# Kernel tuning notes

Measured on AMD Instinct MI355X. Metric: run time of the kernel, lower is better.

The kernel has to match this reference:

```python
import jax, jax.numpy as jnp
import numpy as np

N, F_IN, H, O = 4096, 512, 4, 256
ALPHA = 0.2  # leaky-relu negative slope
NEG = -9e15  # mask value for non-edges (matches DAEGC)


def setup_inputs() -> dict:
    key = jax.random.key(0)
    ks = jax.random.split(key, 9)
    x = jax.random.normal(ks[0], (N, F_IN), jnp.float32)
    adj = (jax.random.uniform(ks[1], (N, N)) < 0.01).astype(jnp.float32)
    adj = jnp.maximum(adj, jnp.eye(N, dtype=jnp.float32))
    M = jax.random.uniform(ks[2], (N, N), dtype=jnp.float32)  # proximity matrix
    s0 = 1.0 / np.sqrt(F_IN)
    s1 = 1.0 / np.sqrt(H * O)
    W0 = jax.random.normal(ks[3], (H, F_IN, O), jnp.float32) * s0
    a_self0 = jax.random.normal(ks[4], (H, O), jnp.float32) * 0.1
    a_neigh0 = jax.random.normal(ks[5], (H, O), jnp.float32) * 0.1
    W1 = jax.random.normal(ks[6], (H, H * O, O), jnp.float32) * s1
    a_self1 = jax.random.normal(ks[7], (H, O), jnp.float32) * 0.1
    a_neigh1 = jax.random.normal(ks[8], (H, O), jnp.float32) * 0.1
    return dict(x=x, adj=adj, M=M, W0=W0, a_self0=a_self0, a_neigh0=a_neigh0,
                W1=W1, a_self1=a_self1, a_neigh1=a_neigh1)


def gat_layer(x, adj, M, W, a_s, a_n, concat):
    # x: [N, F_in], W: [H, F_in, O]
    h = jnp.einsum('nf,hfo->hno', x, W)                      # [H, N, O]
    e = (jnp.einsum('hno,ho->hn', h, a_s)[:, :, None]
         + jnp.einsum('hno,ho->hn', h, a_n)[:, None, :])     # [H, N, N]
    e = jax.nn.leaky_relu(e * M[None], ALPHA)
    e = jnp.where(adj[None] > 0, e, NEG)
    attn = jax.nn.softmax(e, axis=-1)                        # masked neighbor softmax
    out = jnp.einsum('hnm,hmo->hno', attn, h)                # [H, N, O]
    if concat:
        return jax.nn.elu(out.transpose(1, 0, 2).reshape(x.shape[0], -1))  # [N, H*O]
    return out.mean(axis=0)                                  # [N, O]


def reference(x, adj, M, W0, a_self0, a_neigh0, W1, a_self1, a_neigh1):
    h = gat_layer(x, adj, M, W0, a_self0, a_neigh0, True)
    h = gat_layer(h, adj, M, W1, a_self1, a_neigh1, False)
    # F.normalize(h, p=2, dim=1) with eps=1e-12
    z = h / jnp.maximum(jnp.linalg.norm(h, axis=1, keepdims=True), 1e-12)
    A_pred = jax.nn.sigmoid(z @ z.T)                          # dot-product decode [N, N]
    return (A_pred, z)
```

## Files before the change

### kernel.cpp

```cpp
#include <hip/hip_runtime.h>
#include <hip/hip_bf16.h>
#include <math.h>

#define N_NODES 4096
#define F_IN0   512
#define HEADS   4
#define O_DIM   256
#define HO      1024
#define LRELU_A 0.2f
#define MAXE    192
#define LOG2E   1.44269504088896f

typedef __bf16 bf16_t;
typedef bf16_t bf16x8 __attribute__((ext_vector_type(8)));
typedef float f32x4 __attribute__((ext_vector_type(4)));
typedef unsigned short u16x8 __attribute__((ext_vector_type(8)));

__device__ __forceinline__ unsigned short f2b(float f) {
    __hip_bfloat16 t = __float2bfloat16(f);
    return __builtin_bit_cast(unsigned short, t);
}
__device__ __forceinline__ float b2f(unsigned short u) {
    unsigned int v = ((unsigned int)u) << 16;
    return __builtin_bit_cast(float, v);
}
__device__ __forceinline__ float fexp(float x) {
    return __builtin_amdgcn_exp2f(x * LOG2E);
}
__device__ __forceinline__ float fsigmoid(float x) {
    return __builtin_amdgcn_rcpf(1.f + __builtin_amdgcn_exp2f(-x * LOG2E));
}

#define GLOAD_LDS(g, l) \
    __builtin_amdgcn_global_load_lds((const __attribute__((address_space(1))) unsigned int*)(g), \
                                     (__attribute__((address_space(3))) unsigned int*)(l), 16, 0, 0)

__device__ __forceinline__ void transpose_tile(const float* __restrict__ W,
                                               unsigned short* __restrict__ Wt,
                                               int K, int O, int kt, int ot, int h,
                                               float (*t)[33], int tid) {
    const float* Wh = W + (size_t)h * K * O;
    unsigned short* Wth = Wt + (size_t)h * K * O;
    const int k0 = kt * 32, o0 = ot * 32;
    const int tx = tid & 31, ty = tid >> 5;
    for (int r = ty; r < 32; r += 8) t[r][tx] = Wh[(size_t)(k0 + r) * O + o0 + tx];
    __syncthreads();
    for (int r = ty; r < 32; r += 8)
        Wth[(size_t)(o0 + r) * K + k0 + tx] = f2b(t[tx][r]);
}

__global__ __launch_bounds__(256) void prep_k(const float* __restrict__ x,
                                              const float* __restrict__ W0,
                                              const float* __restrict__ W1,
                                              const float* __restrict__ adj,
                                              const float* __restrict__ Mm,
                                              unsigned short* __restrict__ xb,
                                              unsigned short* __restrict__ wt0,
                                              unsigned short* __restrict__ wt1,
                                              int* __restrict__ ecnt,
                                              int* __restrict__ eidx,
                                              float* __restrict__ eMv) {
    __shared__ float t[32][33];
    __shared__ int cnt;
    const int b = blockIdx.x;
    const int tid = threadIdx.x;
    if (b < 2048) {
        int i = b * 256 + tid;
        float4 v = ((const float4*)x)[i];
        ushort4 o;
        o.x = f2b(v.x); o.y = f2b(v.y); o.z = f2b(v.z); o.w = f2b(v.w);
        ((ushort4*)xb)[i] = o;
    } else if (b < 2560) {
        int b2 = b - 2048;
        transpose_tile(W0, wt0, F_IN0, O_DIM, (b2 & 15), ((b2 >> 4) & 7), b2 >> 7, t, tid);
    } else if (b < 3584) {
        int b2 = b - 2560;
        transpose_tile(W1, wt1, HO, O_DIM, (b2 & 31), ((b2 >> 5) & 7), b2 >> 8, t, tid);
    } else {
        const int n = b - 3584;
        if (tid == 0) cnt = 0;
        __syncthreads();
        const float* adjr = adj + (size_t)n * N_NODES;
        const float* Mr   = Mm  + (size_t)n * N_NODES;
        for (int m0 = tid * 4; m0 < N_NODES; m0 += 1024) {
            const float4 a4 = *(const float4*)&adjr[m0];
            const float av[4] = {a4.x, a4.y, a4.z, a4.w};
#pragma unroll
            for (int q = 0; q < 4; ++q) {
                if (av[q] > 0.f) {
                    int m = m0 + q;
                    int k = atomicAdd(&cnt, 1);
                    eidx[(size_t)n * MAXE + k] = m;
                    eMv[(size_t)n * MAXE + k]  = Mr[m];
                }
            }
        }
        __syncthreads();
        if (tid == 0) ecnt[n] = cnt;
    }
}

__global__ __launch_bounds__(256) void mfma_nt(const bf16_t* __restrict__ A,
                                               const bf16_t* __restrict__ B,
                                               unsigned short* __restrict__ Cv,
                                               int K, int ldc,
                                               unsigned long long bStride,
                                               unsigned long long cStride) {
    B += blockIdx.z * bStride;
    const size_t zoff = (size_t)blockIdx.z * cStride;
    __shared__ bf16_t sA[128 * 32];
    __shared__ bf16_t sB[128 * 32];
    const int tid  = threadIdx.x;
    const int lane = tid & 63;
    const int wave = tid >> 6;
    const int wr = (wave >> 1) * 64;
    const int wc = (wave & 1) * 64;
    const int rowBase = blockIdx.x * 128;
    const int colBase = blockIdx.y * 128;
    const int l15  = lane & 15;
    const int quad = lane >> 4;

    const int sm = tid & 127;
    const int sc = tid >> 7;
    const bf16_t* aRow = A + (size_t)(rowBase + sm) * K + sc * 8;
    const bf16_t* bRow = B + (size_t)(colBase + sm) * K + sc * 8;
    bf16_t* sA0 = &sA[(tid & ~63) * 8];
    bf16_t* sA1 = &sA[(256 + (tid & ~63)) * 8];
    bf16_t* sB0 = &sB[(tid & ~63) * 8];
    bf16_t* sB1 = &sB[(256 + (tid & ~63)) * 8];

    f32x4 acc[4][4] = {};

    for (int k0 = 0; k0 < K; k0 += 32) {
        GLOAD_LDS(aRow + k0,      sA0);
        GLOAD_LDS(aRow + k0 + 16, sA1);
        GLOAD_LDS(bRow + k0,      sB0);
        GLOAD_LDS(bRow + k0 + 16, sB1);
        __syncthreads();
        bf16x8 af[4], bfr[4];
#pragma unroll
        for (int i = 0; i < 4; ++i) {
            af[i]  = *(bf16x8*)&sA[(quad * 128 + wr + i * 16 + l15) * 8];
            bfr[i] = *(bf16x8*)&sB[(quad * 128 + wc + i * 16 + l15) * 8];
        }
#pragma unroll
        for (int i = 0; i < 4; ++i)
#pragma unroll
            for (int j = 0; j < 4; ++j)
                acc[i][j] = __builtin_amdgcn_mfma_f32_16x16x32_bf16(af[i], bfr[j], acc[i][j], 0, 0, 0);
        __syncthreads();
    }

    const int orow = rowBase + wr + quad * 4;
    const int ocol = colBase + wc + l15;
#pragma unroll
    for (int i = 0; i < 4; ++i)
#pragma unroll
        for (int j = 0; j < 4; ++j)
#pragma unroll
            for (int r = 0; r < 4; ++r)
                Cv[zoff + (size_t)(orow + i * 16 + r) * ldc + ocol + j * 16] = f2b(acc[i][j][r]);
}

#define EP_STRIDE 132
__global__ __launch_bounds__(256) void decode_k(const bf16_t* __restrict__ Z,
                                                float* __restrict__ out) {
    __shared__ float smem_f[32 * EP_STRIDE];
    bf16_t* sA = (bf16_t*)smem_f;
    bf16_t* sB = (bf16_t*)(smem_f + 2048);
    float*  sE = smem_f;

    const int tid  = threadIdx.x;
    const int lane = tid & 63;
    const int wave = tid >> 6;
    const int wr = (wave >> 1) * 64;
    const int wc = (wave & 1) * 64;
    const int rowBase = blockIdx.x * 128;
    const int colBase = blockIdx.y * 128;
    const int l15  = lane & 15;
    const int quad = lane >> 4;

    const int sm = tid & 127;
    const int sc = tid >> 7;
    const bf16_t* aRow = Z + (size_t)(rowBase + sm) * O_DIM + sc * 8;
    const bf16_t* bRow = Z + (size_t)(colBase + sm) * O_DIM + sc * 8;
    bf16_t* sA0 = &sA[(tid & ~63) * 8];
    bf16_t* sA1 = &sA[(256 + (tid & ~63)) * 8];
    bf16_t* sB0 = &sB[(tid & ~63) * 8];
    bf16_t* sB1 = &sB[(256 + (tid & ~63)) * 8];

    f32x4 acc[4][4] = {};

    for (int k0 = 0; k0 < O_DIM; k0 += 32) {
        GLOAD_LDS(aRow + k0,      sA0);
        GLOAD_LDS(aRow + k0 + 16, sA1);
        GLOAD_LDS(bRow + k0,      sB0);
        GLOAD_LDS(bRow + k0 + 16, sB1);
        __syncthreads();
        bf16x8 af[4], bfr[4];
#pragma unroll
        for (int i = 0; i < 4; ++i) {
            af[i]  = *(bf16x8*)&sA[(quad * 128 + wr + i * 16 + l15) * 8];
            bfr[i] = *(bf16x8*)&sB[(quad * 128 + wc + i * 16 + l15) * 8];
        }
#pragma unroll
        for (int i = 0; i < 4; ++i)
#pragma unroll
            for (int j = 0; j < 4; ++j)
                acc[i][j] = __builtin_amdgcn_mfma_f32_16x16x32_bf16(af[i], bfr[j], acc[i][j], 0, 0, 0);
        __syncthreads();
    }

    const int lrBase = (wave >> 1) * 16;
    for (int i = 0; i < 4; ++i) {
#pragma unroll
        for (int j = 0; j < 4; ++j)
#pragma unroll
            for (int r = 0; r < 4; ++r)
                sE[(lrBase + quad * 4 + r) * EP_STRIDE + wc + j * 16 + l15] = acc[i][j][r];
        __syncthreads();
#pragma unroll
        for (int p = 0; p < 4; ++p) {
            const int idx4 = p * 256 + tid;
            const int lr = idx4 >> 5;
            const int c4 = idx4 & 31;
            f32x4 v = *(f32x4*)&sE[lr * EP_STRIDE + c4 * 4];
            f32x4 o;
            o[0] = fsigmoid(v[0]); o[1] = fsigmoid(v[1]);
            o[2] = fsigmoid(v[2]); o[3] = fsigmoid(v[3]);
            const int grow = rowBase + (lr >> 4) * 64 + i * 16 + (lr & 15);
            *(f32x4*)&out[(size_t)grow * N_NODES + colBase + c4 * 4] = o;
        }
        __syncthreads();
    }
}

__global__ __launch_bounds__(256) void scores_k(const unsigned short* __restrict__ hb,
                                                const float* __restrict__ a_s,
                                                const float* __restrict__ a_n,
                                                float* __restrict__ s_self4,
                                                float* __restrict__ s_neigh4) {
    const int n = blockIdx.x;
    const int head = threadIdx.x >> 6;
    const int lane = threadIdx.x & 63;
    const ushort4 hv = *(const ushort4*)&hb[(size_t)n * HO + head * O_DIM + lane * 4];
    const float4 av = *(const float4*)&a_s[head * O_DIM + lane * 4];
    const float4 nv = *(const float4*)&a_n[head * O_DIM + lane * 4];
    float h0 = b2f(hv.x), h1 = b2f(hv.y), h2 = b2f(hv.z), h3 = b2f(hv.w);
    float ps = h0 * av.x + h1 * av.y + h2 * av.z + h3 * av.w;
    float pn = h0 * nv.x + h1 * nv.y + h2 * nv.z + h3 * nv.w;
    for (int off = 32; off; off >>= 1) {
        ps += __shfl_down(ps, off, 64);
        pn += __shfl_down(pn, off, 64);
    }
    if (lane == 0) {
        s_self4[n * HEADS + head]  = ps;
        s_neigh4[n * HEADS + head] = pn;
    }
}

__global__ __launch_bounds__(256) void attn_k(const unsigned short* __restrict__ hb,
                                              const int* __restrict__ ecnt,
                                              const int* __restrict__ eidx,
                                              const float* __restrict__ eMv,
                                              const float* __restrict__ s_self4,
                                              const float* __restrict__ s_neigh4,
                                              unsigned short* __restrict__ out0,
                                              float* __restrict__ out1, int layer) {
    const int n = blockIdx.x;
    const int tid = threadIdx.x;
    __shared__ int midx[MAXE];
    __shared__ float ev[MAXE][HEADS];
    __shared__ float red2[2][HO];
    const int c = ecnt[n];

    if (tid < c) {
        const int m = eidx[(size_t)n * MAXE + tid];
        const float Mv = eMv[(size_t)n * MAXE + tid];
        midx[tid] = m;
        const float4 ss = *(const float4*)&s_self4[n * HEADS];
        const float4 sn = *(const float4*)&s_neigh4[m * HEADS];
        float e0 = (ss.x + sn.x) * Mv, e1 = (ss.y + sn.y) * Mv;
        float e2 = (ss.z + sn.z) * Mv, e3 = (ss.w + sn.w) * Mv;
        ev[tid][0] = e0 > 0.f ? e0 : LRELU_A * e0;
        ev[tid][1] = e1 > 0.f ? e1 : LRELU_A * e1;
        ev[tid][2] = e2 > 0.f ? e2 : LRELU_A * e2;
        ev[tid][3] = e3 > 0.f ? e3 : LRELU_A * e3;
    }
    __syncthreads();

    {
        const int w = tid >> 6, lane = tid & 63;
        float mx = -1e30f;
        for (int k = lane; k < c; k += 64) mx = fmaxf(mx, ev[k][w]);
        for (int off = 32; off; off >>= 1) mx = fmaxf(mx, __shfl_xor(mx, off, 64));
        float s = 0.f;
        for (int k = lane; k < c; k += 64) {
            float p = fexp(ev[k][w] - mx);
            ev[k][w] = p;
            s += p;
        }
        for (int off = 32; off; off >>= 1) s += __shfl_xor(s, off, 64);
        float inv = __builtin_amdgcn_rcpf(s);
        for (int k = lane; k < c; k += 64) ev[k][w] *= inv;
    }
    __syncthreads();

    const int half = tid >> 7;
    const int t    = tid & 127;
    const int hh   = t >> 5;
    float acc[8] = {};
#pragma unroll 2
    for (int k = half; k < c; k += 2) {
        const int m = midx[k];
        const float w = ev[k][hh];
        const u16x8 hv = *(const u16x8*)&hb[(size_t)m * HO + t * 8];
#pragma unroll
        for (int j = 0; j < 8; ++j) acc[j] += w * b2f(hv[j]);
    }
#pragma unroll
    for (int j = 0; j < 8; ++j) red2[half][t * 8 + j] = acc[j];
    __syncthreads();

    if (layer == 0) {
        const int o = tid * 4;
        ushort4 ov;
        float v0 = red2[0][o + 0] + red2[1][o + 0];
        float v1 = red2[0][o + 1] + red2[1][o + 1];
        float v2 = red2[0][o + 2] + red2[1][o + 2];
        float v3 = red2[0][o + 3] + red2[1][o + 3];
        ov.x = f2b(v0 > 0.f ? v0 : fexp(v0) - 1.f);
        ov.y = f2b(v1 > 0.f ? v1 : fexp(v1) - 1.f);
        ov.z = f2b(v2 > 0.f ? v2 : fexp(v2) - 1.f);
        ov.w = f2b(v3 > 0.f ? v3 : fexp(v3) - 1.f);
        *(ushort4*)&out0[(size_t)n * HO + o] = ov;
    } else {
        const int o = tid;
        float v = 0.f;
#pragma unroll
        for (int h = 0; h < HEADS; ++h)
            v += red2[0][h * O_DIM + o] + red2[1][h * O_DIM + o];
        out1[(size_t)n * O_DIM + o] = 0.25f * v;
    }
}

__global__ __launch_bounds__(256) void norm_k(float* __restrict__ z,
                                              unsigned short* __restrict__ zb) {
    const int n = blockIdx.x;
    const int tid = threadIdx.x;
    float v = z[(size_t)n * O_DIM + tid];
    float p = v * v;
    for (int off = 32; off; off >>= 1) p += __shfl_down(p, off, 64);
    __shared__ float wsum[4];
    if ((tid & 63) == 0) wsum[tid >> 6] = p;
    __syncthreads();
    float ssq = wsum[0] + wsum[1] + wsum[2] + wsum[3];
    float denom = fmaxf(sqrtf(ssq), 1e-12f);
    float zn = v / denom;
    z[(size_t)n * O_DIM + tid] = zn;
    zb[(size_t)n * O_DIM + tid] = f2b(zn);
}

extern "C" void kernel_launch(void* const* d_in, const int* in_sizes, int n_in,
                              void* d_out, int out_size, void* d_ws, size_t ws_size,
                              hipStream_t stream) {
    const float* x   = (const float*)d_in[0];
    const float* adj = (const float*)d_in[1];
    const float* Mm  = (const float*)d_in[2];
    const float* W0  = (const float*)d_in[3];
    const float* as0 = (const float*)d_in[4];
    const float* an0 = (const float*)d_in[5];
    const float* W1  = (const float*)d_in[6];
    const float* as1 = (const float*)d_in[7];
    const float* an1 = (const float*)d_in[8];
    float* out = (float*)d_out;

    unsigned short* hb    = (unsigned short*)d_ws;
    unsigned short* hin1b = hb + (size_t)N_NODES * HO;
    unsigned short* xb    = hin1b + (size_t)N_NODES * HO;
    unsigned short* wt0   = xb + (size_t)N_NODES * F_IN0;
    unsigned short* wt1   = wt0 + HEADS * O_DIM * F_IN0;
    unsigned short* zb    = wt1 + HEADS * O_DIM * HO;
    float* s_self4  = (float*)(zb + (size_t)N_NODES * O_DIM);
    float* s_neigh4 = s_self4 + N_NODES * HEADS;
    int*   eidx = (int*)(s_neigh4 + N_NODES * HEADS);
    float* eMv  = (float*)(eidx + (size_t)N_NODES * MAXE);
    int*   ecnt = (int*)(eMv + (size_t)N_NODES * MAXE);
    float* zbuf = out + (size_t)N_NODES * N_NODES;

    prep_k<<<7680, 256, 0, stream>>>(x, W0, W1, adj, Mm, xb, wt0, wt1, ecnt, eidx, eMv);

    mfma_nt<<<dim3(32, 2, 4), 256, 0, stream>>>((const bf16_t*)xb, (const bf16_t*)wt0, hb,
                                                F_IN0, HO,
                                                (unsigned long long)O_DIM * F_IN0,
                                                (unsigned long long)O_DIM);
    scores_k<<<N_NODES, 256, 0, stream>>>(hb, as0, an0, s_self4, s_neigh4);
    attn_k<<<N_NODES, 256, 0, stream>>>(hb, ecnt, eidx, eMv, s_self4, s_neigh4, hin1b, nullptr, 0);

    mfma_nt<<<dim3(32, 2, 4), 256, 0, stream>>>((const bf16_t*)hin1b, (const bf16_t*)wt1, hb,
                                                HO, HO,
                                                (unsigned long long)O_DIM * HO,
                                                (unsigned long long)O_DIM);
    scores_k<<<N_NODES, 256, 0, stream>>>(hb, as1, an1, s_self4, s_neigh4);
    attn_k<<<N_NODES, 256, 0, stream>>>(hb, ecnt, eidx, eMv, s_self4, s_neigh4, nullptr, zbuf, 1);

    norm_k<<<N_NODES, 256, 0, stream>>>(zbuf, zb);
    decode_k<<<dim3(32, 32), 256, 0, stream>>>((const bf16_t*)zb, out);
}
```

Before: 324.0 us.

## Build edge lists with per-wave ballot-style prefix scan, gather M in attention

Splits adjacency compaction out of the prep kernel into a dedicated edge kernel where each wave handles one row, builds a bitmask, and uses a wave prefix scan to write ordered neighbor indices without shared atomics. The M values are no longer gathered into a compact buffer; attention kernels read M directly at the neighbor index. This removes the block-level atomic contention and one scratch buffer, at the cost of scattered M reads done twice (once per layer) and an extra kernel launch.

```diff
diff --git a/kernel.cpp b/kernel.cpp
--- a/kernel.cpp
+++ b/kernel.cpp
@@ -49,19 +49,13 @@
         Wth[(size_t)(o0 + r) * K + k0 + tx] = f2b(t[tx][r]);
 }
 
-__global__ __launch_bounds__(256) void prep_k(const float* __restrict__ x,
+__global__ __launch_bounds__(256) void conv_k(const float* __restrict__ x,
                                               const float* __restrict__ W0,
                                               const float* __restrict__ W1,
-                                              const float* __restrict__ adj,
-                                              const float* __restrict__ Mm,
                                               unsigned short* __restrict__ xb,
                                               unsigned short* __restrict__ wt0,
-                                              unsigned short* __restrict__ wt1,
-                                              int* __restrict__ ecnt,
-                                              int* __restrict__ eidx,
-                                              float* __restrict__ eMv) {
+                                              unsigned short* __restrict__ wt1) {
     __shared__ float t[32][33];
-    __shared__ int cnt;
     const int b = blockIdx.x;
     const int tid = threadIdx.x;
     if (b < 2048) {
@@ -73,31 +67,48 @@
     } else if (b < 2560) {
         int b2 = b - 2048;
         transpose_tile(W0, wt0, F_IN0, O_DIM, (b2 & 15), ((b2 >> 4) & 7), b2 >> 7, t, tid);
-    } else if (b < 3584) {
+    } else {
         int b2 = b - 2560;
         transpose_tile(W1, wt1, HO, O_DIM, (b2 & 31), ((b2 >> 5) & 7), b2 >> 8, t, tid);
-    } else {
-        const int n = b - 3584;
-        if (tid == 0) cnt = 0;
-        __syncthreads();
-        const float* adjr = adj + (size_t)n * N_NODES;
-        const float* Mr   = Mm  + (size_t)n * N_NODES;
-        for (int m0 = tid * 4; m0 < N_NODES; m0 += 1024) {
-            const float4 a4 = *(const float4*)&adjr[m0];
-            const float av[4] = {a4.x, a4.y, a4.z, a4.w};
-#pragma unroll
-            for (int q = 0; q < 4; ++q) {
-                if (av[q] > 0.f) {
-                    int m = m0 + q;
-                    int k = atomicAdd(&cnt, 1);
-                    eidx[(size_t)n * MAXE + k] = m;
-                    eMv[(size_t)n * MAXE + k]  = Mr[m];
-                }
-            }
-        }
-        __syncthreads();
-        if (tid == 0) ecnt[n] = cnt;
-    }
+    }
+}
+
+__global__ __launch_bounds__(256) void edge_k(const float* __restrict__ adj,
+                                              int* __restrict__ ecnt,
+                                              int* __restrict__ eidx) {
+    const int w    = threadIdx.x >> 6;
+    const int lane = threadIdx.x & 63;
+    const int n    = blockIdx.x * 4 + w;
+    const float* adjr = adj + (size_t)n * N_NODES;
+    float4 a4[16];
+#pragma unroll
+    for (int it = 0; it < 16; ++it)
+        a4[it] = *(const float4*)&adjr[lane * 4 + it * 256];
+    unsigned long long mask = 0;
+#pragma unroll
+    for (int it = 0; it < 16; ++it) {
+        if (a4[it].x > 0.f) mask |= 1ull << (it * 4 + 0);
+        if (a4[it].y > 0.f) mask |= 1ull << (it * 4 + 1);
+        if (a4[it].z > 0.f) mask |= 1ull << (it * 4 + 2);
+        if (a4[it].w > 0.f) mask |= 1ull << (it * 4 + 3);
+    }
+    const int ec = __popcll(mask);
+    int sc = ec;
+#pragma unroll
+    for (int off = 1; off < 64; off <<= 1) {
+        int u = __shfl_up(sc, off, 64);
+        if (lane >= off) sc += u;
+    }
+    int base = sc - ec;
+    unsigned long long mm = mask;
+    while (mm) {
+        const int q = __builtin_ctzll(mm);
+        mm &= mm - 1;
+        const int m = lane * 4 + ((q >> 2) << 8) + (q & 3);
+        eidx[(size_t)n * MAXE + base] = m;
+        ++base;
+    }
+    if (lane == 63) ecnt[n] = sc;
 }
 
 __global__ __launch_bounds__(256) void mfma_nt(const bf16_t* __restrict__ A,
@@ -262,7 +273,7 @@
 __global__ __launch_bounds__(256) void attn_k(const unsigned short* __restrict__ hb,
                                               const int* __restrict__ ecnt,
                                               const int* __restrict__ eidx,
-                                              const float* __restrict__ eMv,
+                                              const float* __restrict__ Mm,
                                               const float* __restrict__ s_self4,
                                               const float* __restrict__ s_neigh4,
                                               unsigned short* __restrict__ out0,
@@ -276,7 +287,7 @@
 
     if (tid < c) {
         const int m = eidx[(size_t)n * MAXE + tid];
-        const float Mv = eMv[(size_t)n * MAXE + tid];
+        const float Mv = Mm[((size_t)n << 12) + m];
         midx[tid] = m;
         const float4 ss = *(const float4*)&s_self4[n * HEADS];
         const float4 sn = *(const float4*)&s_neigh4[m * HEADS];
@@ -384,25 +395,25 @@
     float* s_self4  = (float*)(zb + (size_t)N_NODES * O_DIM);
     float* s_neigh4 = s_self4 + N_NODES * HEADS;
     int*   eidx = (int*)(s_neigh4 + N_NODES * HEADS);
-    float* eMv  = (float*)(eidx + (size_t)N_NODES * MAXE);
-    int*   ecnt = (int*)(eMv + (size_t)N_NODES * MAXE);
+    int*   ecnt = eidx + (size_t)N_NODES * MAXE;
     float* zbuf = out + (size_t)N_NODES * N_NODES;
 
-    prep_k<<<7680, 256, 0, stream>>>(x, W0, W1, adj, Mm, xb, wt0, wt1, ecnt, eidx, eMv);
+    conv_k<<<3584, 256, 0, stream>>>(x, W0, W1, xb, wt0, wt1);
+    edge_k<<<1024, 256, 0, stream>>>(adj, ecnt, eidx);
 
     mfma_nt<<<dim3(32, 2, 4), 256, 0, stream>>>((const bf16_t*)xb, (const bf16_t*)wt0, hb,
                                                 F_IN0, HO,
                                                 (unsigned long long)O_DIM * F_IN0,
                                                 (unsigned long long)O_DIM);
     scores_k<<<N_NODES, 256, 0, stream>>>(hb, as0, an0, s_self4, s_neigh4);
-    attn_k<<<N_NODES, 256, 0, stream>>>(hb, ecnt, eidx, eMv, s_self4, s_neigh4, hin1b, nullptr, 0);
+    attn_k<<<N_NODES, 256, 0, stream>>>(hb, ecnt, eidx, Mm, s_self4, s_neigh4, hin1b, nullptr, 0);
 
     mfma_nt<<<dim3(32, 2, 4), 256, 0, stream>>>((const bf16_t*)hin1b, (const bf16_t*)wt1, hb,
                                                 HO, HO,
                                                 (unsigned long long)O_DIM * HO,
                                                 (unsigned long long)O_DIM);
     scores_k<<<N_NODES, 256, 0, stream>>>(hb, as1, an1, s_self4, s_neigh4);
-    attn_k<<<N_NODES, 256, 0, stream>>>(hb, ecnt, eidx, eMv, s_self4, s_neigh4, nullptr, zbuf, 1);
+    attn_k<<<N_NODES, 256, 0, stream>>>(hb, ecnt, eidx, Mm, s_self4, s_neigh4, nullptr, zbuf, 1);
 
     norm_k<<<N_NODES, 256, 0, stream>>>(zbuf, zb);
     decode_k<<<dim3(32, 32), 256, 0, stream>>>((const bf16_t*)zb, out);
```

After: 322.8 us. About the same (-0.4%).
